# Kernel tuning notes

Measured on AMD Instinct MI355X. Metric: run time of the kernel, lower is better.

The kernel has to match this reference:

```python
import jax, jax.numpy as jnp
import numpy as np

H = 16      # query heads
KV = 4      # kv heads
HD = 128    # head dim
THETA = 10000.0
NEG = -1e9


def _rope_tables(S, dtype):
    inv_freq = 1.0 / (THETA ** (jnp.arange(0, HD, 2, dtype=jnp.float32) / HD))
    ang = jnp.arange(S, dtype=jnp.float32)[:, None] * inv_freq[None, :]  # [S, HD/2]
    emb = jnp.concatenate([ang, ang], axis=-1)  # [S, HD]
    return jnp.cos(emb).astype(dtype), jnp.sin(emb).astype(dtype)


def _rotate_half(x):
    x1, x2 = jnp.split(x, 2, axis=-1)
    return jnp.concatenate([-x2, x1], axis=-1)


def _apply_rope(t, cos, sin):
    # t: [B, h, S, HD]; cos/sin: [S, HD]
    return t * cos[None, None] + _rotate_half(t) * sin[None, None]


def setup_inputs() -> dict:
    key = jax.random.key(0)
    ks = jax.random.split(key, 5)
    B, S, D = 2, 2048, 2048
    sc = 0.02
    return {
        "x": jax.random.normal(ks[0], (B, S, D), jnp.float32),
        "wq": jax.random.normal(ks[1], (D, D), jnp.float32) * sc,
        "wk": jax.random.normal(ks[2], (KV * HD, D), jnp.float32) * sc,
        "wv": jax.random.normal(ks[3], (KV * HD, D), jnp.float32) * sc,
        "wo": jax.random.normal(ks[4], (D, D), jnp.float32) * sc,
    }


def reference(x, wq, wk, wv, wo):
    B, S, D = x.shape
    q = (x @ wq.T).reshape(B, S, H, HD).transpose(0, 2, 1, 3)   # [B,H,S,HD]
    k = (x @ wk.T).reshape(B, S, KV, HD).transpose(0, 2, 1, 3)  # [B,KV,S,HD]
    v = (x @ wv.T).reshape(B, S, KV, HD).transpose(0, 2, 1, 3)

    cos, sin = _rope_tables(S, x.dtype)
    q = _apply_rope(q, cos, sin)
    k = _apply_rope(k, cos, sin)

    # GQA: repeat kv heads to match query heads (q_group_num = H // KV)
    k = jnp.repeat(k, H // KV, axis=1)  # [B,H,S,HD]
    v = jnp.repeat(v, H // KV, axis=1)

    scores = jnp.einsum("bhqd,bhkd->bhqk", q, k) / jnp.sqrt(jnp.float32(HD)).astype(x.dtype)
    causal = jnp.where(jnp.tril(jnp.ones((S, S), bool)), 0.0, NEG).astype(jnp.float32)
    attn = jax.nn.softmax(scores.astype(jnp.float32) + causal, axis=-1).astype(x.dtype)

    out = jnp.einsum("bhqk,bhkd->bhqd", attn, v)  # [B,H,S,HD]
    out = out.transpose(0, 2, 1, 3).reshape(B, S, D)
    return out @ wo.T
```

## Files before the change

### kernel.cpp

```cpp
#include <hip/hip_runtime.h>
#include <math.h>

typedef unsigned short u16;
typedef __attribute__((ext_vector_type(8))) short short8;
typedef __attribute__((ext_vector_type(8))) __bf16 bf16x8;
typedef __attribute__((ext_vector_type(4))) float floatx4;
typedef __attribute__((ext_vector_type(16))) float floatx16;
typedef __attribute__((ext_vector_type(4))) unsigned short u16x4;
typedef __attribute__((ext_vector_type(4))) float float4v;
typedef __attribute__((ext_vector_type(4))) unsigned int uint4v;

static __device__ __forceinline__ float b2f(u16 u) {
  unsigned int x = ((unsigned int)u) << 16;
  return __builtin_bit_cast(float, x);
}
static __device__ __forceinline__ u16 f2b(float f) {
  unsigned int x = __builtin_bit_cast(unsigned int, f);
  x += 0x7fffu + ((x >> 16) & 1u);
  return (u16)(x >> 16);
}
static __device__ __forceinline__ unsigned int pk2(float lo, float hi) {
  unsigned int r;
  asm("v_cvt_pk_bf16_f32 %0, %1, %2" : "=v"(r) : "v"(lo), "v"(hi));
  return r;
}
static __device__ __forceinline__ void gload_lds16(const void* g, void* l) {
  __builtin_amdgcn_global_load_lds(
      (const __attribute__((address_space(1))) unsigned int*)g,
      (__attribute__((address_space(3))) unsigned int*)l, 16, 0, 0);
}

__global__ __launch_bounds__(256) void cvt5_kernel(
    const float* __restrict__ x, const float* __restrict__ wq,
    const float* __restrict__ wk, const float* __restrict__ wv,
    const float* __restrict__ wo, u16* __restrict__ xb, u16* __restrict__ wqb,
    u16* __restrict__ wkb, u16* __restrict__ wvb, u16* __restrict__ wob) {
  int bid = blockIdx.x;
  const float* in;
  u16* out;
  int i0;
  if (bid < 8192) { in = x; out = xb; i0 = bid; }
  else if (bid < 12288) { in = wq; out = wqb; i0 = bid - 8192; }
  else if (bid < 13312) { in = wk; out = wkb; i0 = bid - 12288; }
  else if (bid < 14336) { in = wv; out = wvb; i0 = bid - 13312; }
  else { in = wo; out = wob; i0 = bid - 14336; }
  int i = i0 * 256 + threadIdx.x;
  float4v v = reinterpret_cast<const float4v*>(in)[i];
  u16x4 o;
  o[0] = f2b(v[0]); o[1] = f2b(v[1]); o[2] = f2b(v[2]); o[3] = f2b(v[3]);
  reinterpret_cast<u16x4*>(out)[i] = o;
}

__global__ __launch_bounds__(256) void rope_table_kernel(float* __restrict__ ct,
                                                         float* __restrict__ st) {
  int idx = blockIdx.x * 256 + threadIdx.x;
  int s = idx >> 6, j = idx & 63;
  float inv = powf(10000.0f, -(float)j * (1.0f / 64.0f));
  float ang = (float)s * inv;
  ct[idx] = cosf(ang);
  st[idx] = sinf(ang);
}

__global__ __launch_bounds__(256) void rope_k_kernel(const u16* __restrict__ in,
                                                     u16* __restrict__ out,
                                                     const float* __restrict__ ct,
                                                     const float* __restrict__ st) {
  int idx = blockIdx.x * 256 + threadIdx.x;
  int jc = idx & 7;
  int rest = idx >> 3;
  int h = rest & 3;
  int bs = rest >> 2;
  int s = bs & 2047;
  int b = bs >> 11;
  int j0 = jc * 8;
  size_t inoff = (size_t)bs * 3072 + 2048 + h * 128 + j0;
  short8 lo = *reinterpret_cast<const short8*>(&in[inoff]);
  short8 hi = *reinterpret_cast<const short8*>(&in[inoff + 64]);
  short8 o0, o1;
#pragma unroll
  for (int e = 0; e < 8; ++e) {
    float c = ct[s * 64 + j0 + e], sn = st[s * 64 + j0 + e];
    float t1 = b2f((u16)lo[e]);
    float t2 = b2f((u16)hi[e]);
    o0[e] = (short)f2b(t1 * c - t2 * sn);
    o1[e] = (short)f2b(t2 * c + t1 * sn);
  }
  size_t ooff = ((size_t)(b * 4 + h) * 2048 + s) * 128 + j0;
  *reinterpret_cast<short8*>(&out[ooff]) = o0;
  *reinterpret_cast<short8*>(&out[ooff + 64]) = o1;
}

__global__ __launch_bounds__(256) void vtrans_kernel(const u16* __restrict__ in,
                                                     u16* __restrict__ out) {
  __shared__ u16 t[128][66];
  int s0 = blockIdx.x * 64;
  int b = blockIdx.y >> 2, kv = blockIdx.y & 3;
  int tid = threadIdx.x;
#pragma unroll
  for (int it = 0; it < 32; ++it) {
    int idx = it * 256 + tid;
    int sl = idx >> 7, d = idx & 127;
    t[d][sl] = in[(size_t)(b * 2048 + s0 + sl) * 3072 + 2560 + kv * 128 + d];
  }
  __syncthreads();
#pragma unroll
  for (int it = 0; it < 32; ++it) {
    int idx = it * 256 + tid;
    int d = idx >> 6, sl = idx & 63;
    out[(size_t)((b * 4 + kv) * 128 + d) * 2048 + s0 + sl] = t[d][sl];
  }
}

static __device__ __forceinline__ void store_out(u16* p, float v) { *p = f2b(v); }
static __device__ __forceinline__ void store_out(float* p, float v) { *p = v; }

template <typename OutT>
__global__ __launch_bounds__(256) void gemm_bt(const u16* __restrict__ A,
                                               const u16* __restrict__ B,
                                               OutT* __restrict__ C, int M, int N, int K) {
  __shared__ __align__(16) u16 Al[3][128 * 32];
  __shared__ __align__(16) u16 Bl[3][128 * 32];
  const int tid = threadIdx.x;
  const int lane = tid & 63;
  const int w = tid >> 6;
  const int wr = w >> 1, wc = w & 1;
  const int lr = lane & 15, lg = lane >> 4;
  const int brow = blockIdx.y, bcol = blockIdx.x;
  const int r0 = lane >> 2, kp = lane & 3;
  const u16* Ag = A + (size_t)(brow * 128) * K;
  const u16* Bg = B + (size_t)(bcol * 128) * K;
  floatx4 acc[4][4] = {};
  const int NT = K >> 5;

  auto stage = [&](int buf, int t) {
#pragma unroll
    for (int j = 0; j < 2; ++j) {
      int c = w * 2 + j;
      int row = c * 16 + r0;
      gload_lds16(Ag + (size_t)row * K + t * 32 + kp * 8, &Al[buf][c * 512]);
      gload_lds16(Bg + (size_t)row * K + t * 32 + kp * 8, &Bl[buf][c * 512]);
    }
  };

  stage(0, 0);
  stage(1, 1);
  asm volatile("s_waitcnt vmcnt(4)\n\ts_barrier" ::: "memory");

  int cur = 0, nxt = 2;
  for (int t = 0; t < NT; ++t) {
    if (t + 2 < NT) stage(nxt, t + 2);
    bf16x8 af[4], bfr[4];
#pragma unroll
    for (int m = 0; m < 4; ++m)
      af[m] = *reinterpret_cast<const bf16x8*>(&Al[cur][(wr * 64 + m * 16 + lr) * 32 + lg * 8]);
#pragma unroll
    for (int n = 0; n < 4; ++n)
      bfr[n] = *reinterpret_cast<const bf16x8*>(&Bl[cur][(wc * 64 + n * 16 + lr) * 32 + lg * 8]);
    __builtin_amdgcn_s_setprio(1);
#pragma unroll
    for (int m = 0; m < 4; ++m)
#pragma unroll
      for (int n = 0; n < 4; ++n)
        acc[m][n] = __builtin_amdgcn_mfma_f32_16x16x32_bf16(af[m], bfr[n], acc[m][n], 0, 0, 0);
    __builtin_amdgcn_s_setprio(0);
    if (t + 2 < NT) {
      asm volatile("s_waitcnt vmcnt(4)\n\ts_barrier" ::: "memory");
    } else if (t + 1 < NT) {
      asm volatile("s_waitcnt vmcnt(0)\n\ts_barrier" ::: "memory");
    }
    cur = (cur == 2) ? 0 : cur + 1;
    nxt = (nxt == 2) ? 0 : nxt + 1;
  }
#pragma unroll
  for (int m = 0; m < 4; ++m) {
    int row = brow * 128 + wr * 64 + m * 16 + lg * 4;
#pragma unroll
    for (int n = 0; n < 4; ++n) {
      int col = bcol * 128 + wc * 64 + n * 16 + lr;
#pragma unroll
      for (int i = 0; i < 4; ++i) store_out(&C[(size_t)(row + i) * N + col], acc[m][n][i]);
    }
  }
}

__global__ __launch_bounds__(256, 2) void attn_kernel(
    const u16* __restrict__ QKV, const u16* __restrict__ K,
    const u16* __restrict__ V, const float* __restrict__ ct,
    const float* __restrict__ st, u16* __restrict__ O, u16* __restrict__ Opart,
    float* __restrict__ Mpart, float* __restrict__ Lpart) {
  __shared__ __align__(16) u16 Kl[2][64 * 128];
  __shared__ __align__(16) u16 Vl[2][128 * 64];
  const int tid = threadIdx.x, lane = tid & 63, w = tid >> 6;
  const int ql = lane & 31, h2 = lane >> 5;
  const int idx = blockIdx.x;
  const int bh = idx & 31, pp = (idx >> 5) & 7, half = idx >> 8;
  const int b = bh >> 4, hh = bh & 15, kv = hh >> 2;
  const int t_l = 15 - pp, t_s = pp;
  const int pidx = bh * 8 + pp;
  const u16* Kp = K + (size_t)(b * 4 + kv) * 2048 * 128;
  const u16* Vp = V + (size_t)(b * 4 + kv) * 128 * 2048;
  const float cl = 0.08838834764831845f * 1.44269504088896f;

  auto stage = [&](int buf, int kb) {
#pragma unroll
    for (int j = 0; j < 4; ++j) {
      int slot = j * 256 + tid;
      int row = slot >> 4, d16 = slot & 15;
      gload_lds16(Kp + (size_t)(kb * 64 + row) * 128 + (d16 ^ (row & 15)) * 8,
                  &Kl[buf][(j * 256 + w * 64) * 8]);
      int d = slot >> 3, k8 = slot & 7;
      gload_lds16(Vp + (size_t)d * 2048 + kb * 64 + (k8 ^ (d & 7)) * 8,
                  &Vl[buf][(j * 256 + w * 64) * 8]);
    }
  };

  auto run_segment = [&](int t, int kvs, int kve, int part) {
    const int q0w = t * 128 + w * 32;
    const int qg = q0w + ql;
    bf16x8 qa[8];
    {
      const u16* qp = QKV + ((size_t)(b * 2048 + qg)) * 3072 + hh * 128;
      short8 rr[8];
#pragma unroll
      for (int dk = 0; dk < 8; ++dk)
        rr[dk] = *reinterpret_cast<const short8*>(qp + dk * 16 + h2 * 8);
      const float* cb = ct + (size_t)qg * 64;
      const float* sb = st + (size_t)qg * 64;
#pragma unroll
      for (int dk = 0; dk < 4; ++dk) {
        short8 olo, ohi;
#pragma unroll
        for (int e = 0; e < 8; ++e) {
          int j = dk * 16 + h2 * 8 + e;
          float c = cb[j], sn = sb[j];
          float t1 = b2f((u16)rr[dk][e]);
          float t2 = b2f((u16)rr[dk + 4][e]);
          olo[e] = (short)f2b(t1 * c - t2 * sn);
          ohi[e] = (short)f2b(t2 * c + t1 * sn);
        }
        qa[dk] = __builtin_bit_cast(bf16x8, olo);
        qa[dk + 4] = __builtin_bit_cast(bf16x8, ohi);
      }
    }
    float m_r = -1e30f, l_r = 0.0f;
    floatx16 oacc[4] = {};
    stage(0, kvs);
    __syncthreads();
    int cur = 0;
    for (int kb = kvs; kb < kve; ++kb) {
      if (kb + 1 < kve) stage(cur ^ 1, kb + 1);
      if (kb * 64 <= q0w + 31) {
        const u16* Klc = Kl[cur];
        const u16* Vlc = Vl[cur];
        floatx16 sT0 = {}, sT1 = {};
        __builtin_amdgcn_s_setprio(1);
#pragma unroll
        for (int dk = 0; dk < 8; ++dk) {
          int row0 = ql, row1 = 32 + ql;
          bf16x8 ak0 = *reinterpret_cast<const bf16x8*>(
              &Klc[row0 * 128 + (((dk * 2 + h2) ^ (row0 & 15))) * 8]);
          bf16x8 ak1 = *reinterpret_cast<const bf16x8*>(
              &Klc[row1 * 128 + (((dk * 2 + h2) ^ (row1 & 15))) * 8]);
          sT0 = __builtin_amdgcn_mfma_f32_32x32x16_bf16(ak0, qa[dk], sT0, 0, 0, 0);
          sT1 = __builtin_amdgcn_mfma_f32_32x32x16_bf16(ak1, qa[dk], sT1, 0, 0, 0);
        }
        __builtin_amdgcn_s_setprio(0);
        float x[32];
        const bool domask = (kb * 64 + 63 > q0w);
#pragma unroll
        for (int rg = 0; rg < 16; ++rg) {
          int kloc0 = (rg & 3) + 8 * (rg >> 2) + 4 * h2;
          float v0 = sT0[rg] * cl;
          float v1 = sT1[rg] * cl;
          if (domask) {
            if (kb * 64 + kloc0 > qg) v0 = -1e30f;
            if (kb * 64 + 32 + kloc0 > qg) v1 = -1e30f;
          }
          x[rg] = v0;
          x[16 + rg] = v1;
        }
        float mx[16];
#pragma unroll
        for (int i = 0; i < 16; ++i) mx[i] = fmaxf(x[i], x[i + 16]);
#pragma unroll
        for (int i = 0; i < 8; ++i) mx[i] = fmaxf(mx[i], mx[i + 8]);
#pragma unroll
        for (int i = 0; i < 4; ++i) mx[i] = fmaxf(mx[i], mx[i + 4]);
        float tmax = fmaxf(fmaxf(mx[0], mx[1]), fmaxf(mx[2], mx[3]));
        tmax = fmaxf(tmax, __shfl_xor(tmax, 32));
        if (!__all(tmax - m_r <= 11.0f)) {
          float mn = fmaxf(m_r, tmax);
          float al = exp2f(m_r - mn);
          m_r = mn;
          l_r *= al;
#pragma unroll
          for (int rg = 0; rg < 16; ++rg) {
            int rowq = (rg & 3) + 8 * (rg >> 2) + 4 * h2;
            float arow = __shfl(al, rowq);
            oacc[0][rg] *= arow; oacc[1][rg] *= arow;
            oacc[2][rg] *= arow; oacc[3][rg] *= arow;
          }
        }
        float p[32];
#pragma unroll
        for (int i = 0; i < 32; ++i) p[i] = exp2f(x[i] - m_r);
        float sm[16];
#pragma unroll
        for (int i = 0; i < 16; ++i) sm[i] = p[i] + p[i + 16];
#pragma unroll
        for (int i = 0; i < 8; ++i) sm[i] += sm[i + 8];
#pragma unroll
        for (int i = 0; i < 4; ++i) sm[i] += sm[i + 4];
        float ts = (sm[0] + sm[1]) + (sm[2] + sm[3]);
        ts += __shfl_xor(ts, 32);
        l_r += ts;
        bf16x8 pa[4];
#pragma unroll
        for (int ka = 0; ka < 2; ++ka) {
          const int o = ka * 16;
          unsigned int x0 = pk2(p[o + 0], p[o + 1]);
          unsigned int x1 = pk2(p[o + 2], p[o + 3]);
          unsigned int y0 = pk2(p[o + 4], p[o + 5]);
          unsigned int y1 = pk2(p[o + 6], p[o + 7]);
          asm volatile("v_permlane32_swap_b32 %0, %1" : "+v"(x0), "+v"(y0));
          asm volatile("v_permlane32_swap_b32 %0, %1" : "+v"(x1), "+v"(y1));
          uint4v f0 = {x0, x1, y0, y1};
          pa[ka * 2] = __builtin_bit_cast(bf16x8, f0);
          unsigned int z0 = pk2(p[o + 8], p[o + 9]);
          unsigned int z1 = pk2(p[o + 10], p[o + 11]);
          unsigned int u0 = pk2(p[o + 12], p[o + 13]);
          unsigned int u1 = pk2(p[o + 14], p[o + 15]);
          asm volatile("v_permlane32_swap_b32 %0, %1" : "+v"(z0), "+v"(u0));
          asm volatile("v_permlane32_swap_b32 %0, %1" : "+v"(z1), "+v"(u1));
          uint4v f1 = {z0, z1, u0, u1};
          pa[ka * 2 + 1] = __builtin_bit_cast(bf16x8, f1);
        }
        __builtin_amdgcn_s_setprio(1);
#pragma unroll
        for (int tb = 0; tb < 4; ++tb) {
          int d = tb * 32 + ql;
#pragma unroll
          for (int ks = 0; ks < 4; ++ks) {
            bf16x8 bv = *reinterpret_cast<const bf16x8*>(
                &Vlc[d * 64 + (((ks * 2 + h2) ^ (d & 7))) * 8]);
            oacc[tb] = __builtin_amdgcn_mfma_f32_32x32x16_bf16(pa[ks], bv, oacc[tb], 0, 0, 0);
          }
        }
        __builtin_amdgcn_s_setprio(0);
      }
      __syncthreads();
      cur ^= 1;
    }
    if (part < 0) {
      float linv = 1.0f / l_r;
#pragma unroll
      for (int rg = 0; rg < 16; ++rg) {
        int rowq = (rg & 3) + 8 * (rg >> 2) + 4 * h2;
        float inv = __shfl(linv, rowq);
        int qrow = t * 128 + w * 32 + rowq;
        size_t base = ((size_t)(b * 2048 + qrow)) * 2048 + hh * 128 + ql;
#pragma unroll
        for (int tb = 0; tb < 4; ++tb)
          O[base + tb * 32] = f2b(oacc[tb][rg] * inv);
      }
    } else {
      size_t pb = ((size_t)(part * 256 + pidx)) * 128;
#pragma unroll
      for (int rg = 0; rg < 16; ++rg) {
        int rowq = (rg & 3) + 8 * (rg >> 2) + 4 * h2;
        size_t base = (pb + w * 32 + rowq) * 128 + ql;
#pragma unroll
        for (int tb = 0; tb < 4; ++tb)
          Opart[base + tb * 32] = f2b(oacc[tb][rg]);
      }
      if (h2 == 0) {
        Mpart[pb + w * 32 + ql] = m_r;
        Lpart[pb + w * 32 + ql] = l_r;
      }
    }
  };

  if (half == 0) {
    run_segment(t_l, 0, 17, 0);
  } else {
    run_segment(t_l, 17, 2 * t_l + 2, 1);
    run_segment(t_s, 0, 2 * t_s + 2, -1);
  }
}

__global__ __launch_bounds__(256) void combine_kernel(
    const u16* __restrict__ Opart, const float* __restrict__ Mpart,
    const float* __restrict__ Lpart, u16* __restrict__ O) {
  int pidx = blockIdx.x;
  int bh = pidx >> 3, pp = pidx & 7;
  int b = bh >> 4, hh = bh & 15;
  int t_l = 15 - pp;
  int tid = threadIdx.x;
  int row = tid >> 1, colbase = (tid & 1) * 64;
  size_t pb0 = (size_t)pidx * 128 + row;
  size_t pb1 = (size_t)(256 + pidx) * 128 + row;
  float m0 = Mpart[pb0], m1 = Mpart[pb1];
  float l0 = Lpart[pb0], l1 = Lpart[pb1];
  float M = fmaxf(m0, m1);
  float w0 = exp2f(m0 - M), w1 = exp2f(m1 - M);
  float inv = 1.0f / (w0 * l0 + w1 * l1);
  size_t ob = ((size_t)(b * 2048 + t_l * 128 + row)) * 2048 + hh * 128 + colbase;
#pragma unroll
  for (int k = 0; k < 8; ++k) {
    short8 o0 = *reinterpret_cast<const short8*>(&Opart[pb0 * 128 + colbase + k * 8]);
    short8 o1 = *reinterpret_cast<const short8*>(&Opart[pb1 * 128 + colbase + k * 8]);
    short8 r;
#pragma unroll
    for (int e = 0; e < 8; ++e)
      r[e] = (short)f2b((w0 * b2f((u16)o0[e]) + w1 * b2f((u16)o1[e])) * inv);
    *reinterpret_cast<short8*>(&O[ob + k * 8]) = r;
  }
}

extern "C" void kernel_launch(void* const* d_in, const int* in_sizes, int n_in,
                              void* d_out, int out_size, void* d_ws, size_t ws_size,
                              hipStream_t stream) {
  const float* x  = (const float*)d_in[0];
  const float* wq = (const float*)d_in[1];
  const float* wk = (const float*)d_in[2];
  const float* wv = (const float*)d_in[3];
  const float* wo = (const float*)d_in[4];
  float* out = (float*)d_out;
  char* ws = (char*)d_ws;
  size_t off = 0;
  auto alloc = [&](size_t bytes) -> void* {
    void* p = ws + off;
    off = (off + bytes + 255) & ~(size_t)255;
    return p;
  };
  u16* xb   = (u16*)alloc(4096ull * 2048 * 2);
  u16* wqb  = (u16*)alloc(2048ull * 2048 * 2);
  u16* wkb  = (u16*)alloc(512ull * 2048 * 2);
  u16* wvb  = (u16*)alloc(512ull * 2048 * 2);
  u16* wob  = (u16*)alloc(2048ull * 2048 * 2);
  u16* qkv  = (u16*)alloc(4096ull * 3072 * 2);
  u16* kr   = (u16*)alloc(4096ull * 512 * 2);
  u16* vtb  = (u16*)alloc(4096ull * 512 * 2);
  float* ctab = (float*)alloc(2048ull * 64 * 4);
  float* stab = (float*)alloc(2048ull * 64 * 4);
  u16* opart  = (u16*)alloc(2ull * 256 * 128 * 128 * 2);
  float* mpart = (float*)alloc(2ull * 256 * 128 * 4);
  float* lpart = (float*)alloc(2ull * 256 * 128 * 4);
  u16* attnb = xb;
  (void)in_sizes; (void)n_in; (void)out_size; (void)ws_size;

  cvt5_kernel<<<18432, 256, 0, stream>>>(x, wq, wk, wv, wo, xb, wqb, wkb, wvb, wob);
  rope_table_kernel<<<512, 256, 0, stream>>>(ctab, stab);

  gemm_bt<u16><<<dim3(24, 32), 256, 0, stream>>>(xb, wqb, qkv, 4096, 3072, 2048);

  rope_k_kernel<<<512, 256, 0, stream>>>(qkv, kr, ctab, stab);
  vtrans_kernel<<<dim3(32, 8), 256, 0, stream>>>(qkv, vtb);

  attn_kernel<<<dim3(512), 256, 0, stream>>>(qkv, kr, vtb, ctab, stab, attnb,
                                             opart, mpart, lpart);
  combine_kernel<<<dim3(256), 256, 0, stream>>>(opart, mpart, lpart, attnb);

  gemm_bt<float><<<dim3(16, 32), 256, 0, stream>>>(attnb, wob, out, 4096, 2048, 2048);
}
```

Before: 226.7 us.

## Compute softmax row sums via MFMA with ones vector and fold scale into Q

Replaces the per-lane VALU reduction of softmax probabilities with four extra MFMA ops multiplying the bf16 P fragments by a ones vector, accumulating row sums in a floatx16 that is rescaled together with the output accumulator. The softmax scale is folded into the RoPE cos/sin factors applied to Q, which removes a per-score multiply. The max reduction is also reshaped into three-input max calls. This trades VALU work for matrix-core work and adds 16 accumulator registers. Row sums now come from bf16-rounded probabilities, which slightly changes numerics.

Result: no change. 225.6 us (-0.5%).

```diff
diff --git a/kernel.cpp b/kernel.cpp
--- a/kernel.cpp
+++ b/kernel.cpp
@@ -23,6 +23,9 @@
   unsigned int r;
   asm("v_cvt_pk_bf16_f32 %0, %1, %2" : "=v"(r) : "v"(lo), "v"(hi));
   return r;
+}
+static __device__ __forceinline__ float max3f(float a, float b, float c) {
+  return fmaxf(fmaxf(a, b), c);
 }
 static __device__ __forceinline__ void gload_lds16(const void* g, void* l) {
   __builtin_amdgcn_global_load_lds(
@@ -200,6 +203,8 @@
   const u16* Kp = K + (size_t)(b * 4 + kv) * 2048 * 128;
   const u16* Vp = V + (size_t)(b * 4 + kv) * 128 * 2048;
   const float cl = 0.08838834764831845f * 1.44269504088896f;
+  const uint4v ones_u = {0x3F803F80u, 0x3F803F80u, 0x3F803F80u, 0x3F803F80u};
+  const bf16x8 ones = __builtin_bit_cast(bf16x8, ones_u);
 
   auto stage = [&](int buf, int kb) {
 #pragma unroll
@@ -232,7 +237,7 @@
 #pragma unroll
         for (int e = 0; e < 8; ++e) {
           int j = dk * 16 + h2 * 8 + e;
-          float c = cb[j], sn = sb[j];
+          float c = cb[j] * cl, sn = sb[j] * cl;
           float t1 = b2f((u16)rr[dk][e]);
           float t2 = b2f((u16)rr[dk + 4][e]);
           olo[e] = (short)f2b(t1 * c - t2 * sn);
@@ -242,8 +247,9 @@
         qa[dk + 4] = __builtin_bit_cast(bf16x8, ohi);
       }
     }
-    float m_r = -1e30f, l_r = 0.0f;
+    float m_r = -1e30f;
     floatx16 oacc[4] = {};
+    floatx16 lsum = {};
     stage(0, kvs);
     __syncthreads();
     int cur = 0;
@@ -270,8 +276,8 @@
 #pragma unroll
         for (int rg = 0; rg < 16; ++rg) {
           int kloc0 = (rg & 3) + 8 * (rg >> 2) + 4 * h2;
-          float v0 = sT0[rg] * cl;
-          float v1 = sT1[rg] * cl;
+          float v0 = sT0[rg];
+          float v1 = sT1[rg];
           if (domask) {
             if (kb * 64 + kloc0 > qg) v0 = -1e30f;
             if (kb * 64 + 32 + kloc0 > qg) v1 = -1e30f;
@@ -282,49 +288,40 @@
         float mx[16];
 #pragma unroll
         for (int i = 0; i < 16; ++i) mx[i] = fmaxf(x[i], x[i + 16]);
-#pragma unroll
-        for (int i = 0; i < 8; ++i) mx[i] = fmaxf(mx[i], mx[i + 8]);
-#pragma unroll
-        for (int i = 0; i < 4; ++i) mx[i] = fmaxf(mx[i], mx[i + 4]);
-        float tmax = fmaxf(fmaxf(mx[0], mx[1]), fmaxf(mx[2], mx[3]));
+        float y0 = max3f(mx[0], mx[1], mx[2]);
+        float y1 = max3f(mx[3], mx[4], mx[5]);
+        float y2 = max3f(mx[6], mx[7], mx[8]);
+        float y3 = max3f(mx[9], mx[10], mx[11]);
+        float y4 = max3f(mx[12], mx[13], mx[14]);
+        float tmax = fmaxf(max3f(y0, y1, y2), max3f(y3, y4, mx[15]));
         tmax = fmaxf(tmax, __shfl_xor(tmax, 32));
         if (!__all(tmax - m_r <= 11.0f)) {
           float mn = fmaxf(m_r, tmax);
           float al = exp2f(m_r - mn);
           m_r = mn;
-          l_r *= al;
 #pragma unroll
           for (int rg = 0; rg < 16; ++rg) {
             int rowq = (rg & 3) + 8 * (rg >> 2) + 4 * h2;
             float arow = __shfl(al, rowq);
             oacc[0][rg] *= arow; oacc[1][rg] *= arow;
             oacc[2][rg] *= arow; oacc[3][rg] *= arow;
+            lsum[rg] *= arow;
           }
         }
         float p[32];
 #pragma unroll
         for (int i = 0; i < 32; ++i) p[i] = exp2f(x[i] - m_r);
-        float sm[16];
-#pragma unroll
-        for (int i = 0; i < 16; ++i) sm[i] = p[i] + p[i + 16];
-#pragma unroll
-        for (int i = 0; i < 8; ++i) sm[i] += sm[i + 8];
-#pragma unroll
-        for (int i = 0; i < 4; ++i) sm[i] += sm[i + 4];
-        float ts = (sm[0] + sm[1]) + (sm[2] + sm[3]);
-        ts += __shfl_xor(ts, 32);
-        l_r += ts;
         bf16x8 pa[4];
 #pragma unroll
         for (int ka = 0; ka < 2; ++ka) {
           const int o = ka * 16;
           unsigned int x0 = pk2(p[o + 0], p[o + 1]);
           unsigned int x1 = pk2(p[o + 2], p[o + 3]);
-          unsigned int y0 = pk2(p[o + 4], p[o + 5]);
-          unsigned int y1 = pk2(p[o + 6], p[o + 7]);
-          asm volatile("v_permlane32_swap_b32 %0, %1" : "+v"(x0), "+v"(y0));
-          asm volatile("v_permlane32_swap_b32 %0, %1" : "+v"(x1), "+v"(y1));
-          uint4v f0 = {x0, x1, y0, y1};
+          unsigned int y0u = pk2(p[o + 4], p[o + 5]);
+          unsigned int y1u = pk2(p[o + 6], p[o + 7]);
+          asm volatile("v_permlane32_swap_b32 %0, %1" : "+v"(x0), "+v"(y0u));
+          asm volatile("v_permlane32_swap_b32 %0, %1" : "+v"(x1), "+v"(y1u));
+          uint4v f0 = {x0, x1, y0u, y1u};
           pa[ka * 2] = __builtin_bit_cast(bf16x8, f0);
           unsigned int z0 = pk2(p[o + 8], p[o + 9]);
           unsigned int z1 = pk2(p[o + 10], p[o + 11]);
@@ -346,17 +343,19 @@
             oacc[tb] = __builtin_amdgcn_mfma_f32_32x32x16_bf16(pa[ks], bv, oacc[tb], 0, 0, 0);
           }
         }
+#pragma unroll
+        for (int ks = 0; ks < 4; ++ks)
+          lsum = __builtin_amdgcn_mfma_f32_32x32x16_bf16(pa[ks], ones, lsum, 0, 0, 0);
         __builtin_amdgcn_s_setprio(0);
       }
       __syncthreads();
       cur ^= 1;
     }
     if (part < 0) {
-      float linv = 1.0f / l_r;
 #pragma unroll
       for (int rg = 0; rg < 16; ++rg) {
         int rowq = (rg & 3) + 8 * (rg >> 2) + 4 * h2;
-        float inv = __shfl(linv, rowq);
+        float inv = 1.0f / lsum[rg];
         int qrow = t * 128 + w * 32 + rowq;
         size_t base = ((size_t)(b * 2048 + qrow)) * 2048 + hh * 128 + ql;
 #pragma unroll
@@ -375,7 +374,13 @@
       }
       if (h2 == 0) {
         Mpart[pb + w * 32 + ql] = m_r;
-        Lpart[pb + w * 32 + ql] = l_r;
+      }
+      if (ql == 0) {
+#pragma unroll
+        for (int rg = 0; rg < 16; ++rg) {
+          int rowq = (rg & 3) + 8 * (rg >> 2) + 4 * h2;
+          Lpart[pb + w * 32 + rowq] = lsum[rg];
+        }
       }
     }
   };
```
